# Kernel optimization log

Hardware: AMD Instinct MI355X
Metric: run time of the kernel (lower is better)

The kernel has to match this reference:

```python
import jax, jax.numpy as jnp
import numpy as np

B, M, H = 8, 1024, 1024
NH, HD = 16, 64  # num_heads, head_dim


def setup_inputs() -> dict:
    key = jax.random.key(0)
    ks = jax.random.split(key, 16)
    s = 0.02
    def lin(k, din, dout):
        k1, k2 = jax.random.split(k)
        return (jax.random.normal(k1, (din, dout), jnp.float32) * s,
                jax.random.normal(k2, (dout,), jnp.float32) * s)
    x = jax.random.normal(ks[0], (B, M, H), jnp.float32)
    Wq, bq = lin(ks[1], H, H)
    Wk, bk = lin(ks[2], H, H)
    Wv, bv = lin(ks[3], H, H)
    Wg, bg = lin(ks[4], H, H)
    Wo, bo = lin(ks[5], H, H)
    Wu1, bu1 = lin(ks[6], H, H // 4)
    Wu2, bu2 = lin(ks[7], H // 4, 1)
    return dict(x=x, Wq=Wq, bq=bq, Wk=Wk, bk=bk, Wv=Wv, bv=bv, Wg=Wg, bg=bg,
                Wo=Wo, bo=bo, Wu1=Wu1, bu1=bu1, Wu2=Wu2, bu2=bu2)


def reference(x, Wq, bq, Wk, bk, Wv, bv, Wg, bg, Wo, bo, Wu1, bu1, Wu2, bu2):
    b, m, _ = x.shape
    shp = lambda t: t.reshape(b, m, NH, HD)
    q = shp(x @ Wq + bq)
    k = shp(x @ Wk + bk)
    v = shp(x @ Wv + bv)
    g = jax.nn.sigmoid(shp(x @ Wg + bg))
    scores = jnp.einsum('bmhd,bnhd->bhmn', q, k) / (HD ** 0.5)
    # modality uncertainty: Linear -> ReLU -> Linear -> Softplus, squeeze(-1)
    sigma = jax.nn.softplus(jax.nn.relu(x @ Wu1 + bu1) @ Wu2 + bu2)[..., 0] + 1e-6
    # sigma_pair: [b, 1, m, 1] * [b, 1, 1, m] -> broadcast over heads
    scores = scores / (sigma[:, None, :, None] * sigma[:, None, None, :])
    attn = jax.nn.softmax(scores, axis=-1)
    ctx = jnp.einsum('bhmn,bnhd->bmhd', attn, v) * g
    fused = ctx.reshape(b, m, H)
    z = fused.mean(axis=1) @ Wo + bo
    return (z, attn, sigma)
```

## Files before the change

### kernel.cpp

```cpp
#include <hip/hip_runtime.h>
#include <math.h>

#define BB 8
#define MM 1024
#define HH 1024
#define NH 16
#define HD 64
#define NCAT 4352
#define ROWS (BB*MM)

typedef unsigned short ushortT;
typedef __attribute__((ext_vector_type(8))) short bf16x8;
typedef __attribute__((ext_vector_type(4))) float f32x4;

__device__ __forceinline__ unsigned short f2bf(float f) {
    union { float f; unsigned int u; } v; v.f = f;
    unsigned int u = v.u;
    unsigned int r = (u + 0x7fffu + ((u >> 16) & 1u)) >> 16;
    return (unsigned short)r;
}
__device__ __forceinline__ float bf2f(unsigned short s) {
    union { unsigned int u; float f; } v; v.u = ((unsigned int)s) << 16;
    return v.f;
}

__device__ __forceinline__ void async_copy16(const void* g, void* l) {
    __builtin_amdgcn_global_load_lds(
        (const __attribute__((address_space(1))) unsigned int*)g,
        (__attribute__((address_space(3))) unsigned int*)l, 16, 0, 0);
}

__device__ __forceinline__ bf16x8 lds8(const ushortT* base, int row, int cb) {
    const char* p = (const char*)(base + row * 64);
    return *(const bf16x8*)(p + ((cb * 2) ^ ((row & 7) << 4)));
}

__device__ __forceinline__ void stage_tile(const ushortT* __restrict__ gsrc, size_t rstride,
                                           ushortT* ldst, int wave, int lane) {
#pragma unroll
    for (int i = 0; i < 2; i++) {
        int c = wave * 128 + i * 64 + lane;
        int row = c >> 3;
        int kc = (c & 7) ^ (row & 7);
        async_copy16(&gsrc[(size_t)row * rstride + kc * 8], ldst + c * 8);
    }
}

__global__ void cast_x_k(const float* __restrict__ x, ushortT* __restrict__ Xb) {
    size_t i = ((size_t)blockIdx.x * 256 + threadIdx.x) * 4;
    float4 v = *(const float4*)&x[i];
    ushort4 o;
    o.x = f2bf(v.x); o.y = f2bf(v.y); o.z = f2bf(v.z); o.w = f2bf(v.w);
    *(ushort4*)&Xb[i] = o;
}

__global__ void wtrans_k(const float* __restrict__ Wq, const float* __restrict__ Wk,
                         const float* __restrict__ Wv, const float* __restrict__ Wg,
                         const float* __restrict__ Wu1, ushortT* __restrict__ Wt) {
    __shared__ float t[64][65];
    int n0 = blockIdx.x * 64, k0 = blockIdx.y * 64;
    const float* src; int ncols; int nloc0;
    if (n0 < 1024)      { src = Wq;  nloc0 = n0;        ncols = 1024; }
    else if (n0 < 2048) { src = Wk;  nloc0 = n0 - 1024; ncols = 1024; }
    else if (n0 < 3072) { src = Wv;  nloc0 = n0 - 2048; ncols = 1024; }
    else if (n0 < 4096) { src = Wg;  nloc0 = n0 - 3072; ncols = 1024; }
    else                { src = Wu1; nloc0 = n0 - 4096; ncols = 256;  }
    int tid = threadIdx.x, c = tid & 63, rq = tid >> 6;
#pragma unroll
    for (int i = 0; i < 16; i++) {
        int k = i * 4 + rq;
        t[k][c] = src[(size_t)(k0 + k) * ncols + nloc0 + c];
    }
    __syncthreads();
#pragma unroll
    for (int i = 0; i < 16; i++) {
        int nn = i * 4 + rq;
        Wt[(size_t)(n0 + nn) * 1024 + k0 + c] = f2bf(t[c][nn]);
    }
}

__global__ void biascat_k(const float* __restrict__ bq, const float* __restrict__ bk,
                          const float* __restrict__ bv, const float* __restrict__ bg,
                          const float* __restrict__ bu1, float* __restrict__ bc) {
    int i = blockIdx.x * 256 + threadIdx.x;
    if (i >= NCAT) return;
    float v;
    if (i < 1024) v = bq[i];
    else if (i < 2048) v = bk[i - 1024];
    else if (i < 3072) v = bv[i - 2048];
    else if (i < 4096) v = bg[i - 3072];
    else v = bu1[i - 4096];
    bc[i] = v;
}

__global__ __launch_bounds__(256, 2) void gemm_proj_k(
    const ushortT* __restrict__ Xb, const ushortT* __restrict__ Wt,
    const float* __restrict__ biascat, ushortT* __restrict__ Ycat) {
    __shared__ ushortT lA[128 * 64];
    __shared__ ushortT lB[128 * 64];
    const int tid = threadIdx.x;
    const int wave = tid >> 6;
    const int lane = tid & 63;
    const int quad = lane >> 4;
    const int l16 = lane & 15;
    const int m0 = blockIdx.y * 128;
    const int n0 = blockIdx.x * 128;
    const int wr = (wave >> 1) * 64;
    const int wc = (wave & 1) * 64;

    f32x4 acc[16];
#pragma unroll
    for (int i = 0; i < 16; i++) acc[i] = (f32x4){0.f, 0.f, 0.f, 0.f};

    for (int k0 = 0; k0 < 1024; k0 += 64) {
#pragma unroll
        for (int i = 0; i < 4; i++) {
            int c = wave * 256 + i * 64 + lane;
            int row = c >> 3, kc = c & 7;
            async_copy16(&Xb[(size_t)(m0 + row) * 1024 + k0 + kc * 8], &lA[c * 8]);
            async_copy16(&Wt[(size_t)(n0 + row) * 1024 + k0 + kc * 8], &lB[c * 8]);
        }
        __syncthreads();
#pragma unroll
        for (int kk = 0; kk < 64; kk += 32) {
            bf16x8 a[4], b[4];
#pragma unroll
            for (int i = 0; i < 4; i++)
                a[i] = *(const bf16x8*)&lA[(wr + i * 16 + l16) * 64 + kk + quad * 8];
#pragma unroll
            for (int j = 0; j < 4; j++)
                b[j] = *(const bf16x8*)&lB[(wc + j * 16 + l16) * 64 + kk + quad * 8];
#pragma unroll
            for (int i = 0; i < 4; i++)
#pragma unroll
                for (int j = 0; j < 4; j++)
                    acc[i * 4 + j] = __builtin_amdgcn_mfma_f32_16x16x32_bf16(
                        a[i], b[j], acc[i * 4 + j], 0, 0, 0);
        }
        __syncthreads();
    }

#pragma unroll
    for (int i = 0; i < 4; i++) {
#pragma unroll
        for (int j = 0; j < 4; j++) {
            int col = n0 + wc + j * 16 + l16;
            float bias = biascat[col];
#pragma unroll
            for (int r = 0; r < 4; r++) {
                int row = m0 + wr + i * 16 + quad * 4 + r;
                float y = acc[i * 4 + j][r] + bias;
                if (n0 < 1024) y *= 0.125f;
                else if (n0 < 3072) {  }
                else if (n0 < 4096) y = 1.f / (1.f + __expf(-y));
                else y = fmaxf(y, 0.f);
                Ycat[(size_t)row * NCAT + col] = f2bf(y);
            }
        }
    }
}

__global__ void vtrans_k(const ushortT* __restrict__ Ycat, ushortT* __restrict__ Vt) {
    __shared__ ushortT t[64][72];
    int n0 = blockIdx.x * 64, h = blockIdx.y, b = blockIdx.z;
    const ushortT* Vbase = Ycat + (size_t)(b * MM) * NCAT + 2048 + h * HD;
    int tid = threadIdx.x, c = tid & 63, rq = tid >> 6;
#pragma unroll
    for (int i = 0; i < 16; i++) {
        int n = i * 4 + rq;
        t[n][c] = Vbase[(size_t)(n0 + n) * NCAT + c];
    }
    __syncthreads();
    ushortT* out = Vt + (size_t)((b * NH + h) * HD) * MM;
#pragma unroll
    for (int i = 0; i < 16; i++) {
        int d = i * 4 + rq;
        out[(size_t)d * MM + n0 + c] = t[c][d];
    }
}

__global__ void sigma_k(const ushortT* __restrict__ Ycat, const float* __restrict__ Wu2,
                        const float* __restrict__ bu2, float* __restrict__ out_sigma,
                        float* __restrict__ rsig) {
    int row = blockIdx.x * 4 + (threadIdx.x >> 6);
    int lane = threadIdx.x & 63;
    const ushortT* u = Ycat + (size_t)row * NCAT + 4096;
    ushort4 uv = *(const ushort4*)(u + lane * 4);
    float4 wv = *(const float4*)(Wu2 + lane * 4);
    float acc = bf2f(uv.x) * wv.x + bf2f(uv.y) * wv.y + bf2f(uv.z) * wv.z + bf2f(uv.w) * wv.w;
#pragma unroll
    for (int d = 1; d < 64; d <<= 1) acc += __shfl_xor(acc, d, 64);
    if (lane == 0) {
        float y = acc + bu2[0];
        float sp = (y > 20.f) ? y : log1pf(__expf(y));
        float s = sp + 1e-6f;
        out_sigma[row] = s;
        rsig[row] = 1.f / s;
    }
}

__global__ __launch_bounds__(256, 2) void attn_k(
    const ushortT* __restrict__ Ycat, const ushortT* __restrict__ Vt,
    const float* __restrict__ rsig, float* __restrict__ attn_out,
    float* __restrict__ meanacc) {
    __shared__ ushortT lQ[64 * 64];
    __shared__ ushortT lK[2][64 * 64];
    __shared__ ushortT lV[2][64 * 64];
    __shared__ ushortT lP[4][16 * 64];
    __shared__ float lrs[1024];

    const int tid = threadIdx.x, wave = tid >> 6, lane = tid & 63;
    const int quad = lane >> 4, l16 = lane & 15;
    const int m0 = blockIdx.x * 64, h = blockIdx.y, b = blockIdx.z;

    const ushortT* Qbase = Ycat + (size_t)(b * MM) * NCAT + h * HD;
    const ushortT* Kbase = Ycat + (size_t)(b * MM) * NCAT + 1024 + h * HD;
    const ushortT* Gbase = Ycat + (size_t)(b * MM) * NCAT + 3072 + h * HD;
    const ushortT* Vbase = Vt + (size_t)((b * NH + h) * HD) * MM;

    for (int i = tid; i < 1024; i += 256) lrs[i] = rsig[b * MM + i];
    stage_tile(Qbase + (size_t)m0 * NCAT, NCAT, lQ, wave, lane);
    stage_tile(Kbase, NCAT, lK[0], wave, lane);
    __syncthreads();

    bf16x8 qa[2];
    qa[0] = lds8(lQ, wave * 16 + l16, quad * 8);
    qa[1] = lds8(lQ, wave * 16 + l16, 32 + quad * 8);
    float rm[4];
#pragma unroll
    for (int r = 0; r < 4; r++) rm[r] = lrs[m0 + wave * 16 + quad * 4 + r];

    float L[4] = {0.f, 0.f, 0.f, 0.f};
    int cur = 0;
    for (int n0 = 0; n0 < MM; n0 += 64) {
        if (n0 + 64 < MM)
            stage_tile(Kbase + (size_t)(n0 + 64) * NCAT, NCAT, lK[cur ^ 1], wave, lane);
        const ushortT* Kc = lK[cur];
#pragma unroll
        for (int j = 0; j < 4; j++) {
            bf16x8 b0 = lds8(Kc, j * 16 + l16, quad * 8);
            bf16x8 b1 = lds8(Kc, j * 16 + l16, 32 + quad * 8);
            f32x4 t = (f32x4){0.f, 0.f, 0.f, 0.f};
            t = __builtin_amdgcn_mfma_f32_16x16x32_bf16(qa[0], b0, t, 0, 0, 0);
            t = __builtin_amdgcn_mfma_f32_16x16x32_bf16(qa[1], b1, t, 0, 0, 0);
            float rn = lrs[n0 + j * 16 + l16];
#pragma unroll
            for (int r = 0; r < 4; r++) L[r] += __expf(t[r] * rm[r] * rn);
        }
        __syncthreads();
        cur ^= 1;
    }

    stage_tile(Kbase, NCAT, lK[0], wave, lane);
    stage_tile(Vbase, MM, lV[0], wave, lane);

#pragma unroll
    for (int r = 0; r < 4; r++) {
#pragma unroll
        for (int d = 1; d < 16; d <<= 1) L[r] += __shfl_xor(L[r], d, 16);
    }
    float Li[4];
#pragma unroll
    for (int r = 0; r < 4; r++) Li[r] = 1.f / L[r];

    f32x4 ctx[4];
#pragma unroll
    for (int j = 0; j < 4; j++) ctx[j] = (f32x4){0.f, 0.f, 0.f, 0.f};
    float* attn_base = attn_out + ((size_t)((b * NH + h) * MM + m0)) * MM;
    ushortT* Pw = lP[wave];

    __syncthreads();
    cur = 0;

    for (int n0 = 0; n0 < MM; n0 += 64) {
        if (n0 + 64 < MM) {
            stage_tile(Kbase + (size_t)(n0 + 64) * NCAT, NCAT, lK[cur ^ 1], wave, lane);
            stage_tile(Vbase + (n0 + 64), MM, lV[cur ^ 1], wave, lane);
        }
        const ushortT* Kc = lK[cur];
        const ushortT* Vc = lV[cur];
        float p[4][4];
#pragma unroll
        for (int j = 0; j < 4; j++) {
            bf16x8 b0 = lds8(Kc, j * 16 + l16, quad * 8);
            bf16x8 b1 = lds8(Kc, j * 16 + l16, 32 + quad * 8);
            f32x4 t = (f32x4){0.f, 0.f, 0.f, 0.f};
            t = __builtin_amdgcn_mfma_f32_16x16x32_bf16(qa[0], b0, t, 0, 0, 0);
            t = __builtin_amdgcn_mfma_f32_16x16x32_bf16(qa[1], b1, t, 0, 0, 0);
            float rn = lrs[n0 + j * 16 + l16];
#pragma unroll
            for (int r = 0; r < 4; r++) {
                float pv = __expf(t[r] * rm[r] * rn) * Li[r];
                p[j][r] = pv;
                int prow = quad * 4 + r;
                *(ushortT*)((char*)Pw + prow * 128 +
                            (((j * 16 + l16) * 2) ^ ((prow & 7) << 4))) = f2bf(pv);
            }
        }
#pragma unroll
        for (int j = 0; j < 4; j++)
#pragma unroll
            for (int r = 0; r < 4; r++)
                attn_base[(size_t)(wave * 16 + quad * 4 + r) * MM + n0 + j * 16 + l16] = p[j][r];
        __syncthreads();
#pragma unroll
        for (int kk = 0; kk < 2; kk++) {
            bf16x8 pa = lds8(Pw, l16, kk * 32 + quad * 8);
#pragma unroll
            for (int j = 0; j < 4; j++) {
                bf16x8 vb = lds8(Vc, j * 16 + l16, kk * 32 + quad * 8);
                ctx[j] = __builtin_amdgcn_mfma_f32_16x16x32_bf16(pa, vb, ctx[j], 0, 0, 0);
            }
        }
        __syncthreads();
        cur ^= 1;
    }

#pragma unroll
    for (int j = 0; j < 4; j++) {
        int d = j * 16 + l16;
        float sum = 0.f;
#pragma unroll
        for (int r = 0; r < 4; r++) {
            int mrow = m0 + wave * 16 + quad * 4 + r;
            float gv = bf2f(Gbase[(size_t)mrow * NCAT + d]);
            sum += ctx[j][r] * gv;
        }
        sum += __shfl_xor(sum, 16, 64);
        sum += __shfl_xor(sum, 32, 64);
        if (quad == 0)
            atomicAdd(&meanacc[b * HH + h * HD + d], sum);
    }
}

__global__ void z_k(const float* __restrict__ meanacc, const float* __restrict__ Wo,
                    const float* __restrict__ bo, float* __restrict__ z) {
    int n = blockIdx.x * 256 + threadIdx.x;
    int b = blockIdx.y;
    int k0 = blockIdx.z * 64;
    float acc = 0.f;
#pragma unroll 4
    for (int k = k0; k < k0 + 64; k++)
        acc = fmaf(meanacc[b * HH + k], Wo[(size_t)k * HH + n], acc);
    float v = acc * (1.f / 1024.f);
    if (blockIdx.z == 0) v += bo[n];
    atomicAdd(&z[b * HH + n], v);
}

extern "C" void kernel_launch(void* const* d_in, const int* in_sizes, int n_in,
                              void* d_out, int out_size, void* d_ws, size_t ws_size,
                              hipStream_t stream) {
    const float* x   = (const float*)d_in[0];
    const float* Wq  = (const float*)d_in[1];
    const float* bq  = (const float*)d_in[2];
    const float* Wk  = (const float*)d_in[3];
    const float* bk  = (const float*)d_in[4];
    const float* Wv  = (const float*)d_in[5];
    const float* bv  = (const float*)d_in[6];
    const float* Wg  = (const float*)d_in[7];
    const float* bg  = (const float*)d_in[8];
    const float* Wo  = (const float*)d_in[9];
    const float* bo  = (const float*)d_in[10];
    const float* Wu1 = (const float*)d_in[11];
    const float* bu1 = (const float*)d_in[12];
    const float* Wu2 = (const float*)d_in[13];
    const float* bu2 = (const float*)d_in[14];

    char* ws = (char*)d_ws;
    ushortT* Xb      = (ushortT*)(ws + 0);
    ushortT* Wt      = (ushortT*)(ws + 16777216);
    float*   biascat = (float*)  (ws + 25690112);
    ushortT* Ycat    = (ushortT*)(ws + 25707520);
    ushortT* Vt      = (ushortT*)(ws + 97010688);
    float*   rsig    = (float*)  (ws + 113787904);
    float*   meanacc = (float*)  (ws + 113820672);

    float* z_out     = (float*)d_out;
    float* attn_out  = (float*)d_out + 8192;
    float* sigma_out = (float*)d_out + 8192 + 134217728;

    hipMemsetAsync(z_out, 0, 8192 * sizeof(float), stream);
    hipMemsetAsync(meanacc, 0, 8192 * sizeof(float), stream);

    cast_x_k<<<dim3(ROWS * 1024 / 1024), 256, 0, stream>>>(x, Xb);
    wtrans_k<<<dim3(68, 16), 256, 0, stream>>>(Wq, Wk, Wv, Wg, Wu1, Wt);
    biascat_k<<<dim3(17), 256, 0, stream>>>(bq, bk, bv, bg, bu1, biascat);
    gemm_proj_k<<<dim3(NCAT / 128, ROWS / 128), 256, 0, stream>>>(Xb, Wt, biascat, Ycat);
    vtrans_k<<<dim3(16, NH, BB), 256, 0, stream>>>(Ycat, Vt);
    sigma_k<<<dim3(ROWS / 4), 256, 0, stream>>>(Ycat, Wu2, bu2, sigma_out, rsig);
    attn_k<<<dim3(16, NH, BB), 256, 0, stream>>>(Ycat, Vt, rsig, attn_out, meanacc);
    z_k<<<dim3(4, BB, 16), 256, 0, stream>>>(meanacc, Wo, bo, z_out);
}
```

Before: 863.9 us.

## Double query rows per attention block and single-buffer K/V tiles

After: 882.8 us. 2.2% more time.

```diff
diff --git a/kernel.cpp b/kernel.cpp
--- a/kernel.cpp
+++ b/kernel.cpp
@@ -199,19 +199,17 @@
     }
 }
 
-__global__ __launch_bounds__(256, 2) void attn_k(
+__global__ __launch_bounds__(256, 3) void attn_k(
     const ushortT* __restrict__ Ycat, const ushortT* __restrict__ Vt,
     const float* __restrict__ rsig, float* __restrict__ attn_out,
     float* __restrict__ meanacc) {
-    __shared__ ushortT lQ[64 * 64];
-    __shared__ ushortT lK[2][64 * 64];
-    __shared__ ushortT lV[2][64 * 64];
-    __shared__ ushortT lP[4][16 * 64];
+    __shared__ ushortT lKV[2][64 * 64];
+    __shared__ ushortT lPQ[128 * 64];
     __shared__ float lrs[1024];
 
     const int tid = threadIdx.x, wave = tid >> 6, lane = tid & 63;
     const int quad = lane >> 4, l16 = lane & 15;
-    const int m0 = blockIdx.x * 64, h = blockIdx.y, b = blockIdx.z;
+    const int m0 = blockIdx.x * 128, h = blockIdx.y, b = blockIdx.z;
 
     const ushortT* Qbase = Ycat + (size_t)(b * MM) * NCAT + h * HD;
     const ushortT* Kbase = Ycat + (size_t)(b * MM) * NCAT + 1024 + h * HD;
@@ -219,118 +217,128 @@
     const ushortT* Vbase = Vt + (size_t)((b * NH + h) * HD) * MM;
 
     for (int i = tid; i < 1024; i += 256) lrs[i] = rsig[b * MM + i];
-    stage_tile(Qbase + (size_t)m0 * NCAT, NCAT, lQ, wave, lane);
-    stage_tile(Kbase, NCAT, lK[0], wave, lane);
+#pragma unroll
+    for (int i = 0; i < 4; i++) {
+        int c = wave * 256 + i * 64 + lane;
+        int row = c >> 3, kc = (c & 7) ^ (row & 7);
+        async_copy16(&Qbase[(size_t)(m0 + row) * NCAT + kc * 8], &lPQ[c * 8]);
+    }
+    stage_tile(Kbase, NCAT, lKV[0], wave, lane);
     __syncthreads();
 
-    bf16x8 qa[2];
-    qa[0] = lds8(lQ, wave * 16 + l16, quad * 8);
-    qa[1] = lds8(lQ, wave * 16 + l16, 32 + quad * 8);
-    float rm[4];
-#pragma unroll
-    for (int r = 0; r < 4; r++) rm[r] = lrs[m0 + wave * 16 + quad * 4 + r];
-
-    float L[4] = {0.f, 0.f, 0.f, 0.f};
-    int cur = 0;
+    bf16x8 qa[2][2];
+#pragma unroll
+    for (int rg = 0; rg < 2; rg++)
+#pragma unroll
+        for (int kk = 0; kk < 2; kk++)
+            qa[rg][kk] = lds8(lPQ, wave * 32 + rg * 16 + l16, kk * 32 + quad * 8);
+    float rm[2][4];
+#pragma unroll
+    for (int rg = 0; rg < 2; rg++)
+#pragma unroll
+        for (int r = 0; r < 4; r++)
+            rm[rg][r] = lrs[m0 + wave * 32 + rg * 16 + quad * 4 + r];
+
+    float L[2][4] = {{0.f, 0.f, 0.f, 0.f}, {0.f, 0.f, 0.f, 0.f}};
     for (int n0 = 0; n0 < MM; n0 += 64) {
+#pragma unroll
+        for (int j = 0; j < 4; j++) {
+            bf16x8 b0 = lds8(lKV[0], j * 16 + l16, quad * 8);
+            bf16x8 b1 = lds8(lKV[0], j * 16 + l16, 32 + quad * 8);
+            float rn = lrs[n0 + j * 16 + l16];
+#pragma unroll
+            for (int rg = 0; rg < 2; rg++) {
+                f32x4 t = (f32x4){0.f, 0.f, 0.f, 0.f};
+                t = __builtin_amdgcn_mfma_f32_16x16x32_bf16(qa[rg][0], b0, t, 0, 0, 0);
+                t = __builtin_amdgcn_mfma_f32_16x16x32_bf16(qa[rg][1], b1, t, 0, 0, 0);
+#pragma unroll
+                for (int r = 0; r < 4; r++) L[rg][r] += __expf(t[r] * rm[rg][r] * rn);
+            }
+        }
+        __syncthreads();
         if (n0 + 64 < MM)
-            stage_tile(Kbase + (size_t)(n0 + 64) * NCAT, NCAT, lK[cur ^ 1], wave, lane);
-        const ushortT* Kc = lK[cur];
+            stage_tile(Kbase + (size_t)(n0 + 64) * NCAT, NCAT, lKV[0], wave, lane);
+        __syncthreads();
+    }
+
+    stage_tile(Kbase, NCAT, lKV[0], wave, lane);
+    stage_tile(Vbase, MM, lKV[1], wave, lane);
+#pragma unroll
+    for (int rg = 0; rg < 2; rg++)
+#pragma unroll
+        for (int r = 0; r < 4; r++) {
+            float s = L[rg][r];
+#pragma unroll
+            for (int d = 1; d < 16; d <<= 1) s += __shfl_xor(s, d, 16);
+            L[rg][r] = 1.f / s;
+        }
+
+    f32x4 ctx[2][4];
+#pragma unroll
+    for (int rg = 0; rg < 2; rg++)
+#pragma unroll
+        for (int j = 0; j < 4; j++) ctx[rg][j] = (f32x4){0.f, 0.f, 0.f, 0.f};
+    float* attn_base = attn_out + ((size_t)((b * NH + h) * MM + m0)) * MM;
+    ushortT* Pw = lPQ + wave * 2048;
+    __syncthreads();
+
+    for (int n0 = 0; n0 < MM; n0 += 64) {
+#pragma unroll
+        for (int rg = 0; rg < 2; rg++) {
+#pragma unroll
+            for (int j = 0; j < 4; j++) {
+                bf16x8 b0 = lds8(lKV[0], j * 16 + l16, quad * 8);
+                bf16x8 b1 = lds8(lKV[0], j * 16 + l16, 32 + quad * 8);
+                f32x4 t = (f32x4){0.f, 0.f, 0.f, 0.f};
+                t = __builtin_amdgcn_mfma_f32_16x16x32_bf16(qa[rg][0], b0, t, 0, 0, 0);
+                t = __builtin_amdgcn_mfma_f32_16x16x32_bf16(qa[rg][1], b1, t, 0, 0, 0);
+                float rn = lrs[n0 + j * 16 + l16];
+#pragma unroll
+                for (int r = 0; r < 4; r++) {
+                    float pv = __expf(t[r] * rm[rg][r] * rn) * L[rg][r];
+                    int prow = rg * 16 + quad * 4 + r;
+                    attn_base[(size_t)(wave * 32 + prow) * MM + n0 + j * 16 + l16] = pv;
+                    *(ushortT*)((char*)Pw + prow * 128 +
+                                (((j * 16 + l16) * 2) ^ ((prow & 7) << 4))) = f2bf(pv);
+                }
+            }
+        }
+        __syncthreads();
+#pragma unroll
+        for (int rg = 0; rg < 2; rg++)
+#pragma unroll
+            for (int kk = 0; kk < 2; kk++) {
+                bf16x8 pa = lds8(Pw, rg * 16 + l16, kk * 32 + quad * 8);
+#pragma unroll
+                for (int j = 0; j < 4; j++) {
+                    bf16x8 vb = lds8(lKV[1], j * 16 + l16, kk * 32 + quad * 8);
+                    ctx[rg][j] = __builtin_amdgcn_mfma_f32_16x16x32_bf16(pa, vb, ctx[rg][j], 0, 0, 0);
+                }
+            }
+        __syncthreads();
+        if (n0 + 64 < MM) {
+            stage_tile(Kbase + (size_t)(n0 + 64) * NCAT, NCAT, lKV[0], wave, lane);
+            stage_tile(Vbase + (n0 + 64), MM, lKV[1], wave, lane);
+        }
+        __syncthreads();
+    }
+
+#pragma unroll
+    for (int rg = 0; rg < 2; rg++)
 #pragma unroll
         for (int j = 0; j < 4; j++) {
-            bf16x8 b0 = lds8(Kc, j * 16 + l16, quad * 8);
-            bf16x8 b1 = lds8(Kc, j * 16 + l16, 32 + quad * 8);
-            f32x4 t = (f32x4){0.f, 0.f, 0.f, 0.f};
-            t = __builtin_amdgcn_mfma_f32_16x16x32_bf16(qa[0], b0, t, 0, 0, 0);
-            t = __builtin_amdgcn_mfma_f32_16x16x32_bf16(qa[1], b1, t, 0, 0, 0);
-            float rn = lrs[n0 + j * 16 + l16];
-#pragma unroll
-            for (int r = 0; r < 4; r++) L[r] += __expf(t[r] * rm[r] * rn);
-        }
-        __syncthreads();
-        cur ^= 1;
-    }
-
-    stage_tile(Kbase, NCAT, lK[0], wave, lane);
-    stage_tile(Vbase, MM, lV[0], wave, lane);
-
-#pragma unroll
-    for (int r = 0; r < 4; r++) {
-#pragma unroll
-        for (int d = 1; d < 16; d <<= 1) L[r] += __shfl_xor(L[r], d, 16);
-    }
-    float Li[4];
-#pragma unroll
-    for (int r = 0; r < 4; r++) Li[r] = 1.f / L[r];
-
-    f32x4 ctx[4];
-#pragma unroll
-    for (int j = 0; j < 4; j++) ctx[j] = (f32x4){0.f, 0.f, 0.f, 0.f};
-    float* attn_base = attn_out + ((size_t)((b * NH + h) * MM + m0)) * MM;
-    ushortT* Pw = lP[wave];
-
-    __syncthreads();
-    cur = 0;
-
-    for (int n0 = 0; n0 < MM; n0 += 64) {
-        if (n0 + 64 < MM) {
-            stage_tile(Kbase + (size_t)(n0 + 64) * NCAT, NCAT, lK[cur ^ 1], wave, lane);
-            stage_tile(Vbase + (n0 + 64), MM, lV[cur ^ 1], wave, lane);
-        }
-        const ushortT* Kc = lK[cur];
-        const ushortT* Vc = lV[cur];
-        float p[4][4];
-#pragma unroll
-        for (int j = 0; j < 4; j++) {
-            bf16x8 b0 = lds8(Kc, j * 16 + l16, quad * 8);
-            bf16x8 b1 = lds8(Kc, j * 16 + l16, 32 + quad * 8);
-            f32x4 t = (f32x4){0.f, 0.f, 0.f, 0.f};
-            t = __builtin_amdgcn_mfma_f32_16x16x32_bf16(qa[0], b0, t, 0, 0, 0);
-            t = __builtin_amdgcn_mfma_f32_16x16x32_bf16(qa[1], b1, t, 0, 0, 0);
-            float rn = lrs[n0 + j * 16 + l16];
+            int d = j * 16 + l16;
+            float sum = 0.f;
 #pragma unroll
             for (int r = 0; r < 4; r++) {
-                float pv = __expf(t[r] * rm[r] * rn) * Li[r];
-                p[j][r] = pv;
-                int prow = quad * 4 + r;
-                *(ushortT*)((char*)Pw + prow * 128 +
-                            (((j * 16 + l16) * 2) ^ ((prow & 7) << 4))) = f2bf(pv);
+                int mrow = m0 + wave * 32 + rg * 16 + quad * 4 + r;
+                sum += ctx[rg][j][r] * bf2f(Gbase[(size_t)mrow * NCAT + d]);
             }
-        }
-#pragma unroll
-        for (int j = 0; j < 4; j++)
-#pragma unroll
-            for (int r = 0; r < 4; r++)
-                attn_base[(size_t)(wave * 16 + quad * 4 + r) * MM + n0 + j * 16 + l16] = p[j][r];
-        __syncthreads();
-#pragma unroll
-        for (int kk = 0; kk < 2; kk++) {
-            bf16x8 pa = lds8(Pw, l16, kk * 32 + quad * 8);
-#pragma unroll
-            for (int j = 0; j < 4; j++) {
-                bf16x8 vb = lds8(Vc, j * 16 + l16, kk * 32 + quad * 8);
-                ctx[j] = __builtin_amdgcn_mfma_f32_16x16x32_bf16(pa, vb, ctx[j], 0, 0, 0);
-            }
-        }
-        __syncthreads();
-        cur ^= 1;
-    }
-
-#pragma unroll
-    for (int j = 0; j < 4; j++) {
-        int d = j * 16 + l16;
-        float sum = 0.f;
-#pragma unroll
-        for (int r = 0; r < 4; r++) {
-            int mrow = m0 + wave * 16 + quad * 4 + r;
-            float gv = bf2f(Gbase[(size_t)mrow * NCAT + d]);
-            sum += ctx[j][r] * gv;
-        }
-        sum += __shfl_xor(sum, 16, 64);
-        sum += __shfl_xor(sum, 32, 64);
-        if (quad == 0)
-            atomicAdd(&meanacc[b * HH + h * HD + d], sum);
-    }
+            sum += __shfl_xor(sum, 16, 64);
+            sum += __shfl_xor(sum, 32, 64);
+            if (quad == 0)
+                atomicAdd(&meanacc[b * HH + h * HD + d], sum);
+        }
 }
 
 __global__ void z_k(const float* __restrict__ meanacc, const float* __restrict__ Wo,
@@ -388,6 +396,6 @@
     gemm_proj_k<<<dim3(NCAT / 128, ROWS / 128), 256, 0, stream>>>(Xb, Wt, biascat, Ycat);
     vtrans_k<<<dim3(16, NH, BB), 256, 0, stream>>>(Ycat, Vt);
     sigma_k<<<dim3(ROWS / 4), 256, 0, stream>>>(Ycat, Wu2, bu2, sigma_out, rsig);
-    attn_k<<<dim3(16, NH, BB), 256, 0, stream>>>(Ycat, Vt, rsig, attn_out, meanacc);
+    attn_k<<<dim3(MM / 128, NH, BB), 256, 0, stream>>>(Ycat, Vt, rsig, attn_out, meanacc);
     z_k<<<dim3(4, BB, 16), 256, 0, stream>>>(meanacc, Wo, bo, z_out);
 }
```
